# Kernel optimization log

Measured on AMD Instinct MI355X. Metric: run time of the kernel, lower is better.

## Reference

```python
import jax, jax.numpy as jnp
import numpy as np

D_MODEL = 1024
N_HEADS = 16
HEAD_DIM = D_MODEL // N_HEADS


def setup_inputs() -> dict:
    key = jax.random.key(0)
    k1, k2, k3 = jax.random.split(key, 3)
    B, T = 4, 2048
    x = jax.random.normal(k1, (B, T, D_MODEL), dtype=jnp.float32)
    # torch Linear(d, 3d) weight is [3d, d]; y = x @ W^T. Store as [d, 3d] for x @ W.
    w_qkv = jax.random.normal(k2, (D_MODEL, 3 * D_MODEL), dtype=jnp.float32) * (D_MODEL ** -0.5)
    w_out = jax.random.normal(k3, (D_MODEL, D_MODEL), dtype=jnp.float32) * (D_MODEL ** -0.5)
    return {"x": x, "w_qkv": w_qkv, "w_out": w_out}


def reference(x, w_qkv, w_out):
    B, T, C = x.shape
    qkv = x @ w_qkv                             # [B, T, 3C]
    q, k, v = jnp.split(qkv, 3, axis=2)
    # [B, T, H, Dh] -> work in bthd layout via einsum
    q = q.reshape(B, T, N_HEADS, HEAD_DIM)
    k = k.reshape(B, T, N_HEADS, HEAD_DIM)
    v = v.reshape(B, T, N_HEADS, HEAD_DIM)
    scale = 1.0 / jnp.sqrt(jnp.asarray(HEAD_DIM, dtype=x.dtype))
    attn = jnp.einsum('bqhd,bkhd->bhqk', q, k) * scale   # [B, H, T, T]
    causal = jnp.tril(jnp.ones((T, T), dtype=bool))
    attn = jnp.where(causal, attn, jnp.asarray(-jnp.inf, dtype=attn.dtype))
    attn = jax.nn.softmax(attn, axis=-1)
    out = jnp.einsum('bhqk,bkhd->bqhd', attn, v).reshape(B, T, C)
    return out @ w_out
```

## Files before the change

kernel.cpp:

```cpp
#include <hip/hip_runtime.h>
#include <hip/hip_bf16.h>
#include <cstdint>


typedef __bf16 bf16x8 __attribute__((ext_vector_type(8)));
typedef __bf16 bf16x4 __attribute__((ext_vector_type(4)));
typedef float  f32x4  __attribute__((ext_vector_type(4)));
typedef float  f32x16 __attribute__((ext_vector_type(16)));
typedef unsigned int u32x4 __attribute__((ext_vector_type(4)));
typedef unsigned int u32x2 __attribute__((ext_vector_type(2)));

#define MFMA16(a, b, c) __builtin_amdgcn_mfma_f32_16x16x32_bf16((a), (b), (c), 0, 0, 0)
#define MFMA32(a, b, c) __builtin_amdgcn_mfma_f32_32x32x16_bf16((a), (b), (c), 0, 0, 0)

__device__ __forceinline__ float fexp2(float x) { return __builtin_amdgcn_exp2f(x); }

__device__ __forceinline__ void gload16(const void* g, void* lds) {
  __builtin_amdgcn_global_load_lds(
      (const __attribute__((address_space(1))) void*)(uintptr_t)g,
      (__attribute__((address_space(3))) void*)(uint32_t)(uintptr_t)lds,
      16, 0, 0);
}

__device__ __forceinline__ uint32_t packbf(float a, float b) {
  uint16_t lo = __builtin_bit_cast(uint16_t, (__bf16)a);
  uint16_t hi = __builtin_bit_cast(uint16_t, (__bf16)b);
  return (uint32_t)lo | ((uint32_t)hi << 16);
}

__device__ __forceinline__ float halfswap(float x, int hi) {
  uint32_t u = __builtin_bit_cast(uint32_t, x);
  u32x2 rr = __builtin_amdgcn_permlane32_swap(u, u, false, false);
  return __builtin_bit_cast(float, hi ? rr.x : rr.y);
}

__global__ __launch_bounds__(256) void k_f32_to_bf16(const float* __restrict__ in,
                                                     __bf16* __restrict__ out, int n) {
  int idx = (blockIdx.x * 256 + threadIdx.x) * 4;
  int stride = gridDim.x * 256 * 4;
  for (; idx < n; idx += stride) {
    float4 v = *(const float4*)(in + idx);
    bf16x4 o = { (__bf16)v.x, (__bf16)v.y, (__bf16)v.z, (__bf16)v.w };
    *(bf16x4*)(out + idx) = o;
  }
}

__global__ __launch_bounds__(256) void k_transpose_f32_bf16(const float* __restrict__ in,
                                                            __bf16* __restrict__ out,
                                                            int R, int C, float scale, int nscale) {
  __shared__ float t[64][65];
  const int r0 = blockIdx.y * 64, c0 = blockIdx.x * 64;
  const int tx = threadIdx.x & 15, ty = threadIdx.x >> 4;
#pragma unroll
  for (int rr = 0; rr < 4; ++rr) {
    int r = ty + rr * 16;
    float4 v = *(const float4*)(in + (size_t)(r0 + r) * C + c0 + tx * 4);
    t[r][tx * 4 + 0] = v.x; t[r][tx * 4 + 1] = v.y;
    t[r][tx * 4 + 2] = v.z; t[r][tx * 4 + 3] = v.w;
  }
  __syncthreads();
#pragma unroll
  for (int rr = 0; rr < 4; ++rr) {
    int c = ty + rr * 16;
    float sc = (c0 + c < nscale) ? scale : 1.0f;
    bf16x4 o = { (__bf16)(t[tx * 4 + 0][c] * sc), (__bf16)(t[tx * 4 + 1][c] * sc),
                 (__bf16)(t[tx * 4 + 2][c] * sc), (__bf16)(t[tx * 4 + 3][c] * sc) };
    *(bf16x4*)(out + (size_t)(c0 + c) * R + r0 + tx * 4) = o;
  }
}

template <typename OutT>
__global__ __launch_bounds__(256) void k_gemm_bt(const __bf16* __restrict__ A,
                                                 const __bf16* __restrict__ BT,
                                                 OutT* __restrict__ C,
                                                 int M, int N, int K) {
  __shared__ __align__(16) __bf16 At[128 * 32];
  __shared__ __align__(16) __bf16 Bt[128 * 32];
  const int tid = threadIdx.x;
  const int l = tid & 63, w = tid >> 6;
  const int wr = w >> 1, wc = w & 1;
  const int lr = l & 15, lk = l >> 4;
  const int bm0 = blockIdx.y * 128, bn0 = blockIdx.x * 128;

  const int sm = w * 16 + (l >> 2);
  const int sk = (l & 3) * 8;
  const __bf16* ga0 = A + (size_t)(bm0 + sm) * K + sk;
  const __bf16* ga1 = A + (size_t)(bm0 + 64 + sm) * K + sk;
  const __bf16* gb0 = BT + (size_t)(bn0 + sm) * K + sk;
  const __bf16* gb1 = BT + (size_t)(bn0 + 64 + sm) * K + sk;
  char* lA = (char*)At + w * 1024;
  char* lB = (char*)Bt + w * 1024;

  const f32x4 fz = {0.f, 0.f, 0.f, 0.f};
  f32x4 acc[4][4];
#pragma unroll
  for (int i = 0; i < 4; ++i) {
#pragma unroll
    for (int j = 0; j < 4; ++j) acc[i][j] = fz;
  }

  for (int k0 = 0; k0 < K; k0 += 32) {
    gload16(ga0, lA);
    gload16(ga1, lA + 4096);
    gload16(gb0, lB);
    gload16(gb1, lB + 4096);
    ga0 += 32; ga1 += 32; gb0 += 32; gb1 += 32;
    __syncthreads();
    bf16x8 af[4], bfr[4];
#pragma unroll
    for (int i = 0; i < 4; ++i)
      af[i] = *(const bf16x8*)(At + (wr * 64 + i * 16 + lr) * 32 + lk * 8);
#pragma unroll
    for (int j = 0; j < 4; ++j)
      bfr[j] = *(const bf16x8*)(Bt + (wc * 64 + j * 16 + lr) * 32 + lk * 8);
#pragma unroll
    for (int i = 0; i < 4; ++i) {
#pragma unroll
      for (int j = 0; j < 4; ++j) acc[i][j] = MFMA16(af[i], bfr[j], acc[i][j]);
    }
    __syncthreads();
  }

#pragma unroll
  for (int i = 0; i < 4; ++i) {
#pragma unroll
    for (int j = 0; j < 4; ++j) {
#pragma unroll
      for (int jj = 0; jj < 4; ++jj) {
        int row = bm0 + wr * 64 + i * 16 + lk * 4 + jj;
        int col = bn0 + wc * 64 + j * 16 + lr;
        C[(size_t)row * N + col] = (OutT)acc[i][j][jj];
      }
    }
  }
}

__global__ __launch_bounds__(512, 2) void k_gemm256(const __bf16* __restrict__ A,
                                                    const __bf16* __restrict__ BT,
                                                    __bf16* __restrict__ C,
                                                    __bf16* __restrict__ VT,
                                                    int M, int N, int K) {
  __shared__ __align__(16) __bf16 SMEM[4][2][128 * 64];
  __bf16 (*Als)[2][128 * 64] = &SMEM[0];
  __bf16 (*Bls)[2][128 * 64] = &SMEM[2];
  const int tid = threadIdx.x;
  const int l = tid & 63, w = tid >> 6;
  const int wm = w >> 2, wn = w & 3;
  const int wnh = wn >> 1, wnl = wn & 1;
  const int lr = l & 15, lk = l >> 4, lr7 = lr & 7;
  const int bm0 = blockIdx.y * 256, bn0 = blockIdx.x * 256;
  const int sr0 = w * 8 + (l >> 3);
  const int sc0 = ((l & 7) ^ (l >> 3)) * 8;
  const int xo0 = (lk ^ lr7) * 8;
  const int xo1 = ((4 + lk) ^ lr7) * 8;

#define STAGE_A(KT, H) do {                                                      \
    const __bf16* s_ = A + (size_t)(bm0 + (H) * 128 + sr0) * K + (KT) * 64 + sc0; \
    char* d_ = (char*)&Als[(KT) & 1][H][0] + w * 1024;                            \
    gload16(s_, d_);                                                              \
    gload16(s_ + (size_t)64 * K, d_ + 8192);                                      \
  } while (0)
#define STAGE_B(KT, H) do {                                                       \
    const __bf16* s_ = BT + (size_t)(bn0 + (H) * 128 + sr0) * K + (KT) * 64 + sc0; \
    char* d_ = (char*)&Bls[(KT) & 1][H][0] + w * 1024;                             \
    gload16(s_, d_);                                                               \
    gload16(s_ + (size_t)64 * K, d_ + 8192);                                       \
  } while (0)
#define LDA(SLOT, QM) do {                                                  \
    _Pragma("unroll") for (int f_ = 0; f_ < 4; ++f_) {                      \
      const __bf16* rp_ = &Als[SLOT][wm][0] + ((QM) * 64 + f_ * 16 + lr) * 64; \
      af[f_][0] = *(const bf16x8*)(rp_ + xo0);                              \
      af[f_][1] = *(const bf16x8*)(rp_ + xo1);                              \
    }                                                                       \
  } while (0)
#define LDB(SLOT, QN) do {                                                  \
    _Pragma("unroll") for (int g_ = 0; g_ < 2; ++g_) {                      \
      const __bf16* rp_ = &Bls[SLOT][wnh][0] + (wnl * 64 + (QN) * 32 + g_ * 16 + lr) * 64; \
      bq[QN][g_][0] = *(const bf16x8*)(rp_ + xo0);                          \
      bq[QN][g_][1] = *(const bf16x8*)(rp_ + xo1);                          \
    }                                                                       \
  } while (0)
#define MFMAQ(QM, QN) do {                                                  \
    __builtin_amdgcn_s_setprio(1);                                          \
    _Pragma("unroll") for (int f_ = 0; f_ < 4; ++f_) {                      \
      _Pragma("unroll") for (int g_ = 0; g_ < 2; ++g_) {                    \
        acc[(QM) * 4 + f_][(QN) * 2 + g_] =                                 \
            MFMA16(af[f_][0], bq[QN][g_][0], acc[(QM) * 4 + f_][(QN) * 2 + g_]); \
        acc[(QM) * 4 + f_][(QN) * 2 + g_] =                                 \
            MFMA16(af[f_][1], bq[QN][g_][1], acc[(QM) * 4 + f_][(QN) * 2 + g_]); \
      }                                                                     \
    }                                                                       \
    __builtin_amdgcn_s_setprio(0);                                          \
  } while (0)
#define BAR() asm volatile("s_barrier" ::: "memory")
#define VMCNT2() asm volatile("s_waitcnt vmcnt(2)" ::: "memory")
#define VMCNT0() asm volatile("s_waitcnt vmcnt(0)" ::: "memory")

  f32x4 acc[8][4];
  const f32x4 fz = {0.f, 0.f, 0.f, 0.f};
#pragma unroll
  for (int m = 0; m < 8; ++m) {
#pragma unroll
    for (int n = 0; n < 4; ++n) acc[m][n] = fz;
  }
  bf16x8 af[4][2], bq[2][2][2];

  STAGE_A(0, 0); STAGE_A(0, 1); STAGE_B(0, 0); STAGE_B(0, 1); STAGE_A(1, 0);
  VMCNT2();
  BAR();

  const int NT = K >> 7;
#pragma unroll 1
  for (int t = 0; t < NT; ++t) {
    const int k1 = 2 * t + 1, k2 = 2 * t + 2, k3 = 2 * t + 3;
    const bool last = (t == NT - 1);
    LDA(0, 0); LDB(0, 0);
    STAGE_A(k1, 1);
    BAR(); MFMAQ(0, 0); BAR();
    LDB(0, 1);
    STAGE_B(k1, 0);
    BAR(); MFMAQ(0, 1); BAR();
    LDA(0, 1);
    STAGE_B(k1, 1);
    BAR(); MFMAQ(1, 1); BAR();
    if (!last) { STAGE_A(k2, 0); VMCNT2(); } else { VMCNT0(); }
    BAR(); MFMAQ(1, 0); BAR();
    LDA(1, 0); LDB(1, 0);
    if (!last) STAGE_A(k2, 1);
    BAR(); MFMAQ(0, 0); BAR();
    LDB(1, 1);
    if (!last) STAGE_B(k2, 0);
    BAR(); MFMAQ(0, 1); BAR();
    LDA(1, 1);
    if (!last) STAGE_B(k2, 1);
    BAR(); MFMAQ(1, 1); BAR();
    if (!last) { STAGE_A(k3, 0); VMCNT2(); }
    BAR(); MFMAQ(1, 0); BAR();
  }

  if (VT != nullptr && bn0 >= 2048) {
    __bf16* tb = &SMEM[0][0][0];
    const int LDT = 264;
    const int bb = bm0 >> 11, tbase = bm0 & 2047;
#pragma unroll 1
    for (int hp = 0; hp < 2; ++hp) {
      if (wnh == hp) {
#pragma unroll
        for (int m = 0; m < 8; ++m) {
          const int tt = wm * 128 + (m >> 2) * 64 + (m & 3) * 16 + lk * 4;
#pragma unroll
          for (int n = 0; n < 4; ++n) {
            const int lcol = wnl * 64 + (n >> 1) * 32 + (n & 1) * 16 + lr;
            bf16x4 o = { (__bf16)acc[m][n][0], (__bf16)acc[m][n][1],
                         (__bf16)acc[m][n][2], (__bf16)acc[m][n][3] };
            *(bf16x4*)(tb + lcol * LDT + tt) = o;
          }
        }
      }
      __syncthreads();
#pragma unroll
      for (int it = 0; it < 8; ++it) {
        const int slot = it * 512 + tid;
        const int r = slot >> 5, toff = (slot & 31) * 8;
        bf16x8 v = *(const bf16x8*)(tb + r * LDT + toff);
        const int vcol = (bn0 - 2048) + hp * 128 + r;
        const int hc = vcol >> 6, d = vcol & 63;
        *(bf16x8*)(VT + ((size_t)((bb * 16 + hc) * 64 + d)) * 2048 + tbase + toff) = v;
      }
      if (hp == 0) __syncthreads();
    }
  } else {
#pragma unroll
    for (int m = 0; m < 8; ++m) {
      const int row = bm0 + wm * 128 + (m >> 2) * 64 + (m & 3) * 16 + lk * 4;
#pragma unroll
      for (int n = 0; n < 4; ++n) {
        const int col = bn0 + wn * 64 + (n >> 1) * 32 + (n & 1) * 16 + lr;
#pragma unroll
        for (int jj = 0; jj < 4; ++jj)
          C[(size_t)(row + jj) * N + col] = (__bf16)acc[m][n][jj];
      }
    }
  }
#undef STAGE_A
#undef STAGE_B
#undef LDA
#undef LDB
#undef MFMAQ
#undef BAR
#undef VMCNT2
#undef VMCNT0
}

__global__ __launch_bounds__(256, 2) void k_attn(const __bf16* __restrict__ qkv,
                                                 const __bf16* __restrict__ vt,
                                                 __bf16* __restrict__ ctx) {
  const int id = blockIdx.x;
  const int wg = (id & 7) * 64 + (id >> 3);
  const int p  = wg & 7;
  const int hb = wg >> 3;
  const int h = hb & 15, b = hb >> 4;

  const int l = threadIdx.x & 63, w = threadIdx.x >> 6;
  const int q = l & 31, hi = l >> 5, l7 = l & 7;

  __shared__ __align__(16) __bf16 KVs[3][2][64 * 64];

  const int srow = w * 8 + (l >> 3);
  const int scol = ((l & 7) ^ (l >> 3)) * 8;

  const __bf16* gK0 = qkv + (size_t)(b * 2048 + srow) * 3072 + 1024 + h * 64 + scol;
  const __bf16* gV0 = vt + ((size_t)((b * 16 + h) * 64 + srow)) * 2048 + scol;

  const float NEG = -1e30f;

#pragma unroll 1
  for (int ti = 0; ti < 2; ++ti) {
    const int qb = ti ? p : 15 - p;
    const int q0w = qb * 128 + w * 32;
    const int qg = q0w + q;
    const int nkv = 2 * qb + 2;
    const int kvlast = (q0w + 31) >> 6;

    const __bf16* qp = qkv + (size_t)(b * 2048 + qg) * 3072 + h * 64 + hi * 8;
    bf16x8 qf[4];
#pragma unroll
    for (int d0 = 0; d0 < 4; ++d0) qf[d0] = *(const bf16x8*)(qp + d0 * 16);

    float m_run = NEG, lsum = 0.f;
    f32x16 o0 = (f32x16)(0.0f), o1 = (f32x16)(0.0f);

    const __bf16* kp = gK0;
    const __bf16* vp = gV0;
    auto STG = [&](int buf) {
      char* dK = (char*)&KVs[buf][0][0] + w * 1024;
      char* dV = (char*)&KVs[buf][1][0] + w * 1024;
      gload16(kp, dK);
      gload16(kp + (size_t)32 * 3072, dK + 4096);
      gload16(vp, dV);
      gload16(vp + (size_t)32 * 2048, dV + 4096);
      kp += (size_t)64 * 3072;
      vp += 64;
    };

    STG(0);
    int cur = 0;

#pragma unroll 1
    for (int kvt = 0; kvt < nkv; ++kvt) {
      const int nxt = (cur == 2) ? 0 : cur + 1;
      const int kv0 = kvt * 64;
      if (kvt + 1 < nkv) {
        STG(nxt);
        asm volatile("s_waitcnt vmcnt(4)" ::: "memory");
      } else {
        asm volatile("s_waitcnt vmcnt(0)" ::: "memory");
      }
      asm volatile("s_barrier" ::: "memory");

      if (kvt <= kvlast) {
        const __bf16* Kb = &KVs[cur][0][0];
        const __bf16* Vb = &KVs[cur][1][0];

        f32x16 s0 = (f32x16)(0.0f), s1 = (f32x16)(0.0f);
        __builtin_amdgcn_s_setprio(1);
#pragma unroll
        for (int d0 = 0; d0 < 4; ++d0) {
          bf16x8 k0 = *(const bf16x8*)(Kb + (size_t)q * 64 + (((d0 * 2 + hi) ^ l7) * 8));
          bf16x8 k1 = *(const bf16x8*)(Kb + (size_t)(32 + q) * 64 + (((d0 * 2 + hi) ^ l7) * 8));
          s0 = MFMA32(k0, qf[d0], s0);
          s1 = MFMA32(k1, qf[d0], s1);
        }
        __builtin_amdgcn_s_setprio(0);

        if (kvt == kvlast) {
#pragma unroll
          for (int r = 0; r < 16; ++r) {
            const int kl = (r & 3) + 8 * (r >> 2) + 4 * hi;
            if (kv0 + kl > qg) s0[r] = NEG;
            if (kv0 + 32 + kl > qg) s1[r] = NEG;
          }
        }

        float t[8];
#pragma unroll
        for (int i = 0; i < 8; ++i)
          t[i] = fmaxf(fmaxf(s0[i], s0[i + 8]), fmaxf(s1[i], s1[i + 8]));
#pragma unroll
        for (int i = 0; i < 4; ++i) t[i] = fmaxf(t[i], t[i + 4]);
        float mt = fmaxf(fmaxf(t[0], t[1]), fmaxf(t[2], t[3]));
        mt = fmaxf(mt, halfswap(mt, hi));

        if (!__all(mt - m_run <= 8.0f)) {
          const float al = fexp2(m_run - mt);
          lsum *= al;
#pragma unroll
          for (int r = 0; r < 16; ++r) { o0[r] *= al; o1[r] *= al; }
          m_run = mt;
        }

#pragma unroll
        for (int r = 0; r < 16; ++r) {
          s0[r] = fexp2(s0[r] - m_run);
          s1[r] = fexp2(s1[r] - m_run);
        }
        float sa[8];
#pragma unroll
        for (int i = 0; i < 8; ++i) sa[i] = (s0[i] + s0[i + 8]) + (s1[i] + s1[i + 8]);
#pragma unroll
        for (int i = 0; i < 4; ++i) sa[i] += sa[i + 4];
        float sm = (sa[0] + sa[1]) + (sa[2] + sa[3]);
        sm += halfswap(sm, hi);
        lsum += sm;

        uint32_t c0[8], c1[8];
#pragma unroll
        for (int j = 0; j < 8; ++j) {
          c0[j] = packbf(s0[2 * j], s0[2 * j + 1]);
          c1[j] = packbf(s1[2 * j], s1[2 * j + 1]);
        }
        u32x4 pk[4];
        {
          u32x2 r0 = __builtin_amdgcn_permlane32_swap(c0[0], c0[2], false, false);
          u32x2 r1 = __builtin_amdgcn_permlane32_swap(c0[1], c0[3], false, false);
          u32x2 r2 = __builtin_amdgcn_permlane32_swap(c0[4], c0[6], false, false);
          u32x2 r3 = __builtin_amdgcn_permlane32_swap(c0[5], c0[7], false, false);
          pk[0].x = r0.x; pk[0].y = r1.x; pk[0].z = r0.y; pk[0].w = r1.y;
          pk[1].x = r2.x; pk[1].y = r3.x; pk[1].z = r2.y; pk[1].w = r3.y;
          u32x2 r4 = __builtin_amdgcn_permlane32_swap(c1[0], c1[2], false, false);
          u32x2 r5 = __builtin_amdgcn_permlane32_swap(c1[1], c1[3], false, false);
          u32x2 r6 = __builtin_amdgcn_permlane32_swap(c1[4], c1[6], false, false);
          u32x2 r7 = __builtin_amdgcn_permlane32_swap(c1[5], c1[7], false, false);
          pk[2].x = r4.x; pk[2].y = r5.x; pk[2].z = r4.y; pk[2].w = r5.y;
          pk[3].x = r6.x; pk[3].y = r7.x; pk[3].z = r6.y; pk[3].w = r7.y;
        }
        bf16x8 pf[4];
#pragma unroll
        for (int kc = 0; kc < 4; ++kc) pf[kc] = __builtin_bit_cast(bf16x8, pk[kc]);

        __builtin_amdgcn_s_setprio(1);
#pragma unroll
        for (int kc = 0; kc < 4; ++kc) {
          bf16x8 vf0 = *(const bf16x8*)(Vb + (size_t)q * 64 + (((kc * 2 + hi) ^ l7) * 8));
          o0 = MFMA32(vf0, pf[kc], o0);
        }
#pragma unroll
        for (int kc = 0; kc < 4; ++kc) {
          bf16x8 vf1 = *(const bf16x8*)(Vb + (size_t)(32 + q) * 64 + (((kc * 2 + hi) ^ l7) * 8));
          o1 = MFMA32(vf1, pf[kc], o1);
        }
        __builtin_amdgcn_s_setprio(0);
      }
      cur = nxt;
    }
    __syncthreads();

    const float inv = 1.0f / lsum;
    __bf16* Ol = &KVs[0][0][0];
#pragma unroll
    for (int r = 0; r < 16; ++r) {
      const int d = (r & 3) + 8 * (r >> 2) + 4 * hi;
      Ol[(w * 32 + q) * 72 + d]      = (__bf16)(o0[r] * inv);
      Ol[(w * 32 + q) * 72 + 32 + d] = (__bf16)(o1[r] * inv);
    }
    __syncthreads();
    {
      const int row = threadIdx.x >> 1, half = threadIdx.x & 1;
      const __bf16* src = Ol + row * 72 + half * 32;
      __bf16* dst = ctx + (size_t)(b * 2048 + qb * 128 + row) * 1024 + h * 64 + half * 32;
#pragma unroll
      for (int i = 0; i < 4; ++i)
        *(bf16x8*)(dst + i * 8) = *(const bf16x8*)(src + i * 8);
    }
    __syncthreads();
  }
}

extern "C" void kernel_launch(void* const* d_in, const int* in_sizes, int n_in,
                              void* d_out, int out_size, void* d_ws, size_t ws_size,
                              hipStream_t stream) {
  const float* x    = (const float*)d_in[0];
  const float* wqkv = (const float*)d_in[1];
  const float* wout = (const float*)d_in[2];
  float* out = (float*)d_out;

  char* ws = (char*)d_ws;
  __bf16* xb    = (__bf16*)(ws);
  __bf16* wqkvT = (__bf16*)(ws + 16777216);
  __bf16* woutT = (__bf16*)(ws + 23068672);
  __bf16* qkvb  = (__bf16*)(ws + 25165824);
  __bf16* vtb   = (__bf16*)(ws + 75497472);
  __bf16* ctx   = (__bf16*)(ws + 92274688);

  const float qscale = 0.125f * 1.44269504088896340736f;

  k_f32_to_bf16<<<2048, 256, 0, stream>>>(x, xb, 8192 * 1024);
  k_transpose_f32_bf16<<<dim3(48, 16), 256, 0, stream>>>(wqkv, wqkvT, 1024, 3072, qscale, 1024);
  k_transpose_f32_bf16<<<dim3(16, 16), 256, 0, stream>>>(wout, woutT, 1024, 1024, 1.0f, 0);
  k_gemm256<<<dim3(12, 32), 512, 0, stream>>>(xb, wqkvT, qkvb, vtb, 8192, 3072, 1024);
  k_attn<<<512, 256, 0, stream>>>(qkvb, vtb, ctx);
  k_gemm_bt<float><<<dim3(8, 64), 256, 0, stream>>>(ctx, woutT, out, 8192, 1024, 1024);
}
```

Measured before the change: 170.3 us.

## Swizzle GEMM LDS, compute softmax row sums via MFMA, unroll KV ring loop

Four independent changes. The GEMM kernel XOR-swizzles its LDS layout to avoid bank conflicts on fragment reads. The attention kernel unrolls the three-buffer KV loop so buffer indices are compile-time constants. It replaces the VALU/permlane row-sum reduction with an extra MFMA against a ones vector, accumulating the softmax denominator in the matrix unit. It also uses the v_cvt_pk_bf16_f32 instruction for packing. The trade-off is extra MFMA work, a 16-register accumulator, and sums taken from bf16-rounded probabilities rather than fp32.

```diff
diff --git a/kernel.cpp b/kernel.cpp
--- a/kernel.cpp
+++ b/kernel.cpp
@@ -22,10 +22,10 @@
       16, 0, 0);
 }
 
-__device__ __forceinline__ uint32_t packbf(float a, float b) {
-  uint16_t lo = __builtin_bit_cast(uint16_t, (__bf16)a);
-  uint16_t hi = __builtin_bit_cast(uint16_t, (__bf16)b);
-  return (uint32_t)lo | ((uint32_t)hi << 16);
+__device__ __forceinline__ uint32_t cvtpk(float a, float b) {
+  uint32_t r;
+  asm("v_cvt_pk_bf16_f32 %0, %1, %2" : "=v"(r) : "v"(a), "v"(b));
+  return r;
 }
 
 __device__ __forceinline__ float halfswap(float x, int hi) {
@@ -83,7 +83,8 @@
   const int bm0 = blockIdx.y * 128, bn0 = blockIdx.x * 128;
 
   const int sm = w * 16 + (l >> 2);
-  const int sk = (l & 3) * 8;
+  const int sk = ((l & 3) ^ ((l >> 3) & 3)) * 8;
+  const int xko = (lk ^ ((lr >> 1) & 3)) * 8;
   const __bf16* ga0 = A + (size_t)(bm0 + sm) * K + sk;
   const __bf16* ga1 = A + (size_t)(bm0 + 64 + sm) * K + sk;
   const __bf16* gb0 = BT + (size_t)(bn0 + sm) * K + sk;
@@ -109,10 +110,10 @@
     bf16x8 af[4], bfr[4];
 #pragma unroll
     for (int i = 0; i < 4; ++i)
-      af[i] = *(const bf16x8*)(At + (wr * 64 + i * 16 + lr) * 32 + lk * 8);
+      af[i] = *(const bf16x8*)(At + (wr * 64 + i * 16 + lr) * 32 + xko);
 #pragma unroll
     for (int j = 0; j < 4; ++j)
-      bfr[j] = *(const bf16x8*)(Bt + (wc * 64 + j * 16 + lr) * 32 + lk * 8);
+      bfr[j] = *(const bf16x8*)(Bt + (wc * 64 + j * 16 + lr) * 32 + xko);
 #pragma unroll
     for (int i = 0; i < 4; ++i) {
 #pragma unroll
@@ -314,6 +315,104 @@
 
   const float NEG = -1e30f;
 
+  bf16x8 ones;
+#pragma unroll
+  for (int i = 0; i < 8; ++i) ones[i] = (__bf16)1.0f;
+
+#define STG(BUF) do {                                                        \
+    char* dK_ = (char*)&KVs[BUF][0][0] + w * 1024;                           \
+    char* dV_ = (char*)&KVs[BUF][1][0] + w * 1024;                           \
+    gload16(kp, dK_);                                                        \
+    gload16(kp + (size_t)32 * 3072, dK_ + 4096);                             \
+    gload16(vp, dV_);                                                        \
+    gload16(vp + (size_t)32 * 2048, dV_ + 4096);                             \
+    kp += (size_t)64 * 3072;                                                 \
+    vp += 64;                                                                \
+  } while (0)
+
+#define ATTN_TILE(BUF, NXT) do {                                             \
+    const int kv0 = kvt * 64;                                                \
+    if (kvt + 1 < nkv) {                                                     \
+      STG(NXT);                                                              \
+      asm volatile("s_waitcnt vmcnt(4)" ::: "memory");                       \
+    } else {                                                                 \
+      asm volatile("s_waitcnt vmcnt(0)" ::: "memory");                       \
+    }                                                                        \
+    asm volatile("s_barrier" ::: "memory");                                  \
+    if (kvt <= kvlast) {                                                     \
+      const __bf16* Kb = &KVs[BUF][0][0];                                    \
+      const __bf16* Vb = &KVs[BUF][1][0];                                    \
+      f32x16 s0 = (f32x16)(0.0f), s1 = (f32x16)(0.0f);                       \
+      __builtin_amdgcn_s_setprio(1);                                         \
+      _Pragma("unroll") for (int d0 = 0; d0 < 4; ++d0) {                     \
+        bf16x8 k0 = *(const bf16x8*)(Kb + (size_t)q * 64 + (((d0 * 2 + hi) ^ l7) * 8)); \
+        bf16x8 k1 = *(const bf16x8*)(Kb + (size_t)(32 + q) * 64 + (((d0 * 2 + hi) ^ l7) * 8)); \
+        s0 = MFMA32(k0, qf[d0], s0);                                         \
+        s1 = MFMA32(k1, qf[d0], s1);                                         \
+      }                                                                      \
+      __builtin_amdgcn_s_setprio(0);                                         \
+      if (kvt == kvlast) {                                                   \
+        _Pragma("unroll") for (int r = 0; r < 16; ++r) {                     \
+          const int kl = (r & 3) + 8 * (r >> 2) + 4 * hi;                    \
+          if (kv0 + kl > qg) s0[r] = NEG;                                    \
+          if (kv0 + 32 + kl > qg) s1[r] = NEG;                               \
+        }                                                                    \
+      }                                                                      \
+      float t[8];                                                            \
+      _Pragma("unroll") for (int i = 0; i < 8; ++i)                          \
+        t[i] = fmaxf(fmaxf(s0[i], s0[i + 8]), fmaxf(s1[i], s1[i + 8]));      \
+      _Pragma("unroll") for (int i = 0; i < 4; ++i) t[i] = fmaxf(t[i], t[i + 4]); \
+      float mt = fmaxf(fmaxf(t[0], t[1]), fmaxf(t[2], t[3]));                \
+      mt = fmaxf(mt, halfswap(mt, hi));                                      \
+      if (!__all(mt - m_run <= 8.0f)) {                                      \
+        const float al = fexp2(m_run - mt);                                  \
+        _Pragma("unroll") for (int r = 0; r < 16; ++r) {                     \
+          o0[r] *= al; o1[r] *= al; os[r] *= al;                             \
+        }                                                                    \
+        m_run = mt;                                                          \
+      }                                                                      \
+      _Pragma("unroll") for (int r = 0; r < 16; ++r) {                       \
+        s0[r] = fexp2(s0[r] - m_run);                                        \
+        s1[r] = fexp2(s1[r] - m_run);                                        \
+      }                                                                      \
+      uint32_t c0[8], c1[8];                                                 \
+      _Pragma("unroll") for (int j = 0; j < 8; ++j) {                        \
+        c0[j] = cvtpk(s0[2 * j], s0[2 * j + 1]);                             \
+        c1[j] = cvtpk(s1[2 * j], s1[2 * j + 1]);                             \
+      }                                                                      \
+      u32x4 pk[4];                                                           \
+      {                                                                      \
+        u32x2 r0 = __builtin_amdgcn_permlane32_swap(c0[0], c0[2], false, false); \
+        u32x2 r1 = __builtin_amdgcn_permlane32_swap(c0[1], c0[3], false, false); \
+        u32x2 r2 = __builtin_amdgcn_permlane32_swap(c0[4], c0[6], false, false); \
+        u32x2 r3 = __builtin_amdgcn_permlane32_swap(c0[5], c0[7], false, false); \
+        pk[0].x = r0.x; pk[0].y = r1.x; pk[0].z = r0.y; pk[0].w = r1.y;      \
+        pk[1].x = r2.x; pk[1].y = r3.x; pk[1].z = r2.y; pk[1].w = r3.y;      \
+        u32x2 r4 = __builtin_amdgcn_permlane32_swap(c1[0], c1[2], false, false); \
+        u32x2 r5 = __builtin_amdgcn_permlane32_swap(c1[1], c1[3], false, false); \
+        u32x2 r6 = __builtin_amdgcn_permlane32_swap(c1[4], c1[6], false, false); \
+        u32x2 r7 = __builtin_amdgcn_permlane32_swap(c1[5], c1[7], false, false); \
+        pk[2].x = r4.x; pk[2].y = r5.x; pk[2].z = r4.y; pk[2].w = r5.y;      \
+        pk[3].x = r6.x; pk[3].y = r7.x; pk[3].z = r6.y; pk[3].w = r7.y;      \
+      }                                                                      \
+      bf16x8 pf[4];                                                          \
+      _Pragma("unroll") for (int kc = 0; kc < 4; ++kc)                       \
+        pf[kc] = __builtin_bit_cast(bf16x8, pk[kc]);                         \
+      __builtin_amdgcn_s_setprio(1);                                         \
+      _Pragma("unroll") for (int kc = 0; kc < 4; ++kc) {                     \
+        bf16x8 vf0 = *(const bf16x8*)(Vb + (size_t)q * 64 + (((kc * 2 + hi) ^ l7) * 8)); \
+        o0 = MFMA32(vf0, pf[kc], o0);                                        \
+      }                                                                      \
+      _Pragma("unroll") for (int kc = 0; kc < 4; ++kc) {                     \
+        bf16x8 vf1 = *(const bf16x8*)(Vb + (size_t)(32 + q) * 64 + (((kc * 2 + hi) ^ l7) * 8)); \
+        o1 = MFMA32(vf1, pf[kc], o1);                                        \
+      }                                                                      \
+      _Pragma("unroll") for (int kc = 0; kc < 4; ++kc)                       \
+        os = MFMA32(ones, pf[kc], os);         \
+      __builtin_amdgcn_s_setprio(0);                                         \
+    }                                                                        \
+  } while (0)
+
 #pragma unroll 1
   for (int ti = 0; ti < 2; ++ti) {
     const int qb = ti ? p : 15 - p;
@@ -327,135 +426,22 @@
 #pragma unroll
     for (int d0 = 0; d0 < 4; ++d0) qf[d0] = *(const bf16x8*)(qp + d0 * 16);
 
-    float m_run = NEG, lsum = 0.f;
-    f32x16 o0 = (f32x16)(0.0f), o1 = (f32x16)(0.0f);
+    float m_run = NEG;
+    f32x16 o0 = (f32x16)(0.0f), o1 = (f32x16)(0.0f), os = (f32x16)(0.0f);
 
     const __bf16* kp = gK0;
     const __bf16* vp = gV0;
-    auto STG = [&](int buf) {
-      char* dK = (char*)&KVs[buf][0][0] + w * 1024;
-      char* dV = (char*)&KVs[buf][1][0] + w * 1024;
-      gload16(kp, dK);
-      gload16(kp + (size_t)32 * 3072, dK + 4096);
-      gload16(vp, dV);
-      gload16(vp + (size_t)32 * 2048, dV + 4096);
-      kp += (size_t)64 * 3072;
-      vp += 64;
-    };
 
     STG(0);
-    int cur = 0;
-
-#pragma unroll 1
-    for (int kvt = 0; kvt < nkv; ++kvt) {
-      const int nxt = (cur == 2) ? 0 : cur + 1;
-      const int kv0 = kvt * 64;
-      if (kvt + 1 < nkv) {
-        STG(nxt);
-        asm volatile("s_waitcnt vmcnt(4)" ::: "memory");
-      } else {
-        asm volatile("s_waitcnt vmcnt(0)" ::: "memory");
-      }
-      asm volatile("s_barrier" ::: "memory");
-
-      if (kvt <= kvlast) {
-        const __bf16* Kb = &KVs[cur][0][0];
-        const __bf16* Vb = &KVs[cur][1][0];
-
-        f32x16 s0 = (f32x16)(0.0f), s1 = (f32x16)(0.0f);
-        __builtin_amdgcn_s_setprio(1);
-#pragma unroll
-        for (int d0 = 0; d0 < 4; ++d0) {
-          bf16x8 k0 = *(const bf16x8*)(Kb + (size_t)q * 64 + (((d0 * 2 + hi) ^ l7) * 8));
-          bf16x8 k1 = *(const bf16x8*)(Kb + (size_t)(32 + q) * 64 + (((d0 * 2 + hi) ^ l7) * 8));
-          s0 = MFMA32(k0, qf[d0], s0);
-          s1 = MFMA32(k1, qf[d0], s1);
-        }
-        __builtin_amdgcn_s_setprio(0);
-
-        if (kvt == kvlast) {
-#pragma unroll
-          for (int r = 0; r < 16; ++r) {
-            const int kl = (r & 3) + 8 * (r >> 2) + 4 * hi;
-            if (kv0 + kl > qg) s0[r] = NEG;
-            if (kv0 + 32 + kl > qg) s1[r] = NEG;
-          }
-        }
-
-        float t[8];
-#pragma unroll
-        for (int i = 0; i < 8; ++i)
-          t[i] = fmaxf(fmaxf(s0[i], s0[i + 8]), fmaxf(s1[i], s1[i + 8]));
-#pragma unroll
-        for (int i = 0; i < 4; ++i) t[i] = fmaxf(t[i], t[i + 4]);
-        float mt = fmaxf(fmaxf(t[0], t[1]), fmaxf(t[2], t[3]));
-        mt = fmaxf(mt, halfswap(mt, hi));
-
-        if (!__all(mt - m_run <= 8.0f)) {
-          const float al = fexp2(m_run - mt);
-          lsum *= al;
-#pragma unroll
-          for (int r = 0; r < 16; ++r) { o0[r] *= al; o1[r] *= al; }
-          m_run = mt;
-        }
-
-#pragma unroll
-        for (int r = 0; r < 16; ++r) {
-          s0[r] = fexp2(s0[r] - m_run);
-          s1[r] = fexp2(s1[r] - m_run);
-        }
-        float sa[8];
-#pragma unroll
-        for (int i = 0; i < 8; ++i) sa[i] = (s0[i] + s0[i + 8]) + (s1[i] + s1[i + 8]);
-#pragma unroll
-        for (int i = 0; i < 4; ++i) sa[i] += sa[i + 4];
-        float sm = (sa[0] + sa[1]) + (sa[2] + sa[3]);
-        sm += halfswap(sm, hi);
-        lsum += sm;
-
-        uint32_t c0[8], c1[8];
-#pragma unroll
-        for (int j = 0; j < 8; ++j) {
-          c0[j] = packbf(s0[2 * j], s0[2 * j + 1]);
-          c1[j] = packbf(s1[2 * j], s1[2 * j + 1]);
-        }
-        u32x4 pk[4];
-        {
-          u32x2 r0 = __builtin_amdgcn_permlane32_swap(c0[0], c0[2], false, false);
-          u32x2 r1 = __builtin_amdgcn_permlane32_swap(c0[1], c0[3], false, false);
-          u32x2 r2 = __builtin_amdgcn_permlane32_swap(c0[4], c0[6], false, false);
-          u32x2 r3 = __builtin_amdgcn_permlane32_swap(c0[5], c0[7], false, false);
-          pk[0].x = r0.x; pk[0].y = r1.x; pk[0].z = r0.y; pk[0].w = r1.y;
-          pk[1].x = r2.x; pk[1].y = r3.x; pk[1].z = r2.y; pk[1].w = r3.y;
-          u32x2 r4 = __builtin_amdgcn_permlane32_swap(c1[0], c1[2], false, false);
-          u32x2 r5 = __builtin_amdgcn_permlane32_swap(c1[1], c1[3], false, false);
-          u32x2 r6 = __builtin_amdgcn_permlane32_swap(c1[4], c1[6], false, false);
-          u32x2 r7 = __builtin_amdgcn_permlane32_swap(c1[5], c1[7], false, false);
-          pk[2].x = r4.x; pk[2].y = r5.x; pk[2].z = r4.y; pk[2].w = r5.y;
-          pk[3].x = r6.x; pk[3].y = r7.x; pk[3].z = r6.y; pk[3].w = r7.y;
-        }
-        bf16x8 pf[4];
-#pragma unroll
-        for (int kc = 0; kc < 4; ++kc) pf[kc] = __builtin_bit_cast(bf16x8, pk[kc]);
-
-        __builtin_amdgcn_s_setprio(1);
-#pragma unroll
-        for (int kc = 0; kc < 4; ++kc) {
-          bf16x8 vf0 = *(const bf16x8*)(Vb + (size_t)q * 64 + (((kc * 2 + hi) ^ l7) * 8));
-          o0 = MFMA32(vf0, pf[kc], o0);
-        }
-#pragma unroll
-        for (int kc = 0; kc < 4; ++kc) {
-          bf16x8 vf1 = *(const bf16x8*)(Vb + (size_t)(32 + q) * 64 + (((kc * 2 + hi) ^ l7) * 8));
-          o1 = MFMA32(vf1, pf[kc], o1);
-        }
-        __builtin_amdgcn_s_setprio(0);
-      }
-      cur = nxt;
+    int kvt = 0;
+    while (true) {
+      ATTN_TILE(0, 1); if (++kvt == nkv) break;
+      ATTN_TILE(1, 2); if (++kvt == nkv) break;
+      ATTN_TILE(2, 0); if (++kvt == nkv) break;
     }
     __syncthreads();
 
-    const float inv = 1.0f / lsum;
+    const float inv = 1.0f / os[0];
     __bf16* Ol = &KVs[0][0][0];
 #pragma unroll
     for (int r = 0; r < 16; ++r) {
@@ -474,6 +460,8 @@
     }
     __syncthreads();
   }
+#undef STG
+#undef ATTN_TILE
 }
 
 extern "C" void kernel_launch(void* const* d_in, const int* in_sizes, int n_in,
```

Result: no change. 167.5 us (-1.6%).
